# Optimization experiments

Measured on AMD Instinct MI355X. Metric: run time of the kernel, lower is better.

## Reference

```python
import jax, jax.numpy as jnp
import numpy as np

N, NUM_MEM, HIDDEN = 131072, 1024, 256
TEMPERATURE = 0.5
EPS = 1e-12  # matches F.normalize default eps


def setup_inputs() -> dict:
    key = jax.random.key(0)
    k1, k2 = jax.random.split(key)
    x = jax.random.normal(k1, (N, HIDDEN), dtype=jnp.float32)
    # xavier_uniform-style init for the memory bank
    limit = float(np.sqrt(6.0 / (NUM_MEM + HIDDEN)))
    memories = jax.random.uniform(k2, (NUM_MEM, HIDDEN), dtype=jnp.float32,
                                  minval=-limit, maxval=limit)
    return {"x": x, "memories": memories}


def reference(x, memories):
    # cosine similarity: normalize both sides, then QK^T
    x_norm = x / jnp.maximum(jnp.linalg.norm(x, axis=-1, keepdims=True), EPS)
    mem_norm = memories / jnp.maximum(
        jnp.linalg.norm(memories, axis=-1, keepdims=True), EPS)
    logits = jnp.einsum('nd,md->nm', x_norm, mem_norm) / TEMPERATURE
    weight = jax.nn.softmax(logits, axis=-1)        # [N, num_memories]
    read = jnp.einsum('nm,md->nd', weight, memories)  # weighted memory read
    return read
```

## Files before the change

kernel.cpp:

```cpp
#include <hip/hip_runtime.h>
#include <hip/hip_bf16.h>
#include <stdint.h>

#define HIDDEN 256
#define NMEM   1024
#define NTILES 32
#define LOG2E  1.44269504088896340736f

typedef __attribute__((ext_vector_type(8)))  short bf16x8;
typedef __attribute__((ext_vector_type(16))) float f32x16;
typedef unsigned short ushort_t;
typedef unsigned int   uint_t;

__device__ __forceinline__ ushort_t f2bf(float f) {
  uint_t u = __builtin_bit_cast(uint_t, f);
  u += 0x7FFFu + ((u >> 16) & 1u);
  return (ushort_t)(u >> 16);
}

__device__ __forceinline__ void gload_lds16(const void* g, void* l) {
  __builtin_amdgcn_global_load_lds(
      (const __attribute__((address_space(1))) uint_t*)g,
      (__attribute__((address_space(3))) uint_t*)l, 16, 0, 0);
}

__global__ void prep_kernel(const float* __restrict__ mem,
                            ushort_t* __restrict__ wsm,
                            ushort_t* __restrict__ wsv) {
  const int m = blockIdx.x;
  const int k = threadIdx.x;
  float v = mem[m * HIDDEN + k];
  float ss = v * v;
  #pragma unroll
  for (int off = 1; off < 64; off <<= 1) ss += __shfl_xor(ss, off);
  __shared__ float red[4];
  if ((k & 63) == 0) red[k >> 6] = ss;
  __syncthreads();
  const float tot = red[0] + red[1] + red[2] + red[3];
  const float inv = 1.0f / fmaxf(sqrtf(tot), 1e-12f);
  const ushort_t hn = f2bf(v * inv);
  const ushort_t hv = f2bf(v);
  const int t = m >> 5, mr = m & 31;
  wsm[t * 8192 + mr * 256 + (((k >> 3) ^ (mr & 7)) << 3) + (k & 7)] = hn;
  wsv[t * 8192 + k * 32  + (((mr >> 3) ^ ((k >> 1) & 3)) << 3) + (mr & 7)] = hv;
}

__global__ __launch_bounds__(512, 2) void mem_kernel(
    const float* __restrict__ x, const ushort_t* __restrict__ wsm,
    const ushort_t* __restrict__ wsv, float* __restrict__ out) {
  __shared__ __align__(16) char lds[65536];
  const int tid  = threadIdx.x;
  const int lane = tid & 63;
  const int wave = tid >> 6;
  const int col  = lane & 31;
  const int hi   = lane >> 5;
  const int row0 = blockIdx.x * 256 + wave * 32;
  const char* gm = (const char*)wsm;
  const char* gv = (const char*)wsv;

  auto stage = [&](int t, int buf) {
    const int bb = buf << 15;
    const int go = t * 16384;
    #pragma unroll
    for (int r = 0; r < 2; ++r) {
      const int o = wave * 2048 + r * 1024;
      gload_lds16(gm + go + o + lane * 16, lds + bb + o);
      gload_lds16(gv + go + o + lane * 16, lds + bb + 16384 + o);
    }
  };

  stage(0, 0);

  bf16x8 xb[16];
  float ss = 0.f;
  const float* xr = x + (size_t)(row0 + col) * HIDDEN + hi * 8;
  #pragma unroll
  for (int ks = 0; ks < 16; ++ks) {
    float4 a = *(const float4*)(xr + ks * 16);
    float4 b = *(const float4*)(xr + ks * 16 + 4);
    ss += a.x*a.x + a.y*a.y + a.z*a.z + a.w*a.w
        + b.x*b.x + b.y*b.y + b.z*b.z + b.w*b.w;
    xb[ks][0] = (short)f2bf(a.x); xb[ks][1] = (short)f2bf(a.y);
    xb[ks][2] = (short)f2bf(a.z); xb[ks][3] = (short)f2bf(a.w);
    xb[ks][4] = (short)f2bf(b.x); xb[ks][5] = (short)f2bf(b.y);
    xb[ks][6] = (short)f2bf(b.z); xb[ks][7] = (short)f2bf(b.w);
  }
  ss += __shfl_xor(ss, 32);
  const float myscale = (2.0f * LOG2E) / fmaxf(sqrtf(ss), 1e-12f);

  const f32x16 zz = {0.f,0.f,0.f,0.f, 0.f,0.f,0.f,0.f,
                     0.f,0.f,0.f,0.f, 0.f,0.f,0.f,0.f};
  f32x16 o8[8];
  #pragma unroll
  for (int i = 0; i < 8; ++i) o8[i] = zz;
  float den = 0.f;

  const int ck7 = col & 7;
  const int ck3 = (col >> 1) & 3;

  __syncthreads();

  for (int t = 0; t < NTILES; ++t) {
    const int mb = (t & 1) << 15;
    const int vb = mb + 16384;
    if (t < NTILES - 1) stage(t + 1, (t & 1) ^ 1);
    __builtin_amdgcn_s_setprio(1);

    const char* ab = lds + mb + col * 512;
    f32x16 s0 = zz, s1 = zz;
    #pragma unroll
    for (int ks2 = 0; ks2 < 8; ++ks2) {
      bf16x8 a0 = *(const bf16x8*)(ab + (((4*ks2 + hi)     ^ ck7) << 4));
      bf16x8 a1 = *(const bf16x8*)(ab + (((4*ks2 + 2 + hi) ^ ck7) << 4));
      s0 = __builtin_amdgcn_mfma_f32_32x32x16_bf16(a0, xb[2*ks2],   s0, 0,0,0);
      s1 = __builtin_amdgcn_mfma_f32_32x32x16_bf16(a1, xb[2*ks2+1], s1, 0,0,0);
    }

    float p[16];
    #pragma unroll
    for (int r = 0; r < 16; ++r) {
      const float pv = exp2f((s0[r] + s1[r]) * myscale);
      den += pv;
      p[r] = pv;
    }

    bf16x8 pa[2];
    #pragma unroll
    for (int ks = 0; ks < 2; ++ks) {
      const int b0 = ks * 8;
      uint_t w0 = (uint_t)f2bf(p[b0+0]) | ((uint_t)f2bf(p[b0+1]) << 16);
      uint_t w1 = (uint_t)f2bf(p[b0+2]) | ((uint_t)f2bf(p[b0+3]) << 16);
      uint_t w2 = (uint_t)f2bf(p[b0+4]) | ((uint_t)f2bf(p[b0+5]) << 16);
      uint_t w3 = (uint_t)f2bf(p[b0+6]) | ((uint_t)f2bf(p[b0+7]) << 16);
      asm("v_permlane32_swap_b32 %0, %1" : "+v"(w0), "+v"(w2));
      asm("v_permlane32_swap_b32 %0, %1" : "+v"(w1), "+v"(w3));
      uint4 u = {w0, w1, w2, w3};
      pa[ks] = __builtin_bit_cast(bf16x8, u);
    }

    const char* vrb = lds + vb + col * 64;
    #pragma unroll
    for (int ks = 0; ks < 2; ++ks) {
      const int cc = ((2*ks + hi) ^ ck3) << 4;
      #pragma unroll
      for (int d0 = 0; d0 < 8; ++d0) {
        bf16x8 vf = *(const bf16x8*)(vrb + d0 * 2048 + cc);
        o8[d0] = __builtin_amdgcn_mfma_f32_32x32x16_bf16(pa[ks], vf, o8[d0], 0,0,0);
      }
    }
    __builtin_amdgcn_s_setprio(0);
    __syncthreads();
  }

  den += __shfl_xor(den, 32);
  const float rden = 1.0f / den;
  float rdv[16];
  #pragma unroll
  for (int r = 0; r < 16; ++r)
    rdv[r] = __shfl(rden, (r & 3) + 8 * (r >> 2) + 4 * hi);

  float* op = out + (size_t)row0 * HIDDEN;
  #pragma unroll
  for (int d0 = 0; d0 < 8; ++d0) {
    #pragma unroll
    for (int r = 0; r < 16; ++r) {
      const int rw = (r & 3) + 8 * (r >> 2) + 4 * hi;
      op[(size_t)rw * HIDDEN + d0 * 32 + col] = o8[d0][r] * rdv[r];
    }
  }
}

extern "C" void kernel_launch(void* const* d_in, const int* in_sizes, int n_in,
                              void* d_out, int out_size, void* d_ws, size_t ws_size,
                              hipStream_t stream) {
  const float* x   = (const float*)d_in[0];
  const float* mem = (const float*)d_in[1];
  float* out = (float*)d_out;
  const int N = in_sizes[0] / HIDDEN;

  ushort_t* wsm = (ushort_t*)d_ws;
  ushort_t* wsv = wsm + NMEM * HIDDEN;

  prep_kernel<<<NMEM, HIDDEN, 0, stream>>>(mem, wsm, wsv);
  mem_kernel<<<N / 256, 512, 0, stream>>>(x, wsm, wsv, out);
}
```

Before: 381.4 us.

## Software-pipeline QK and PV across tiles with triple-buffered LDS

Restructures the main loop so each iteration runs the QK MFMAs for the current tile while issuing the PV MFMAs for the previous tile's packed probabilities. A third LDS buffer is added so the PV operands of the previous tile stay resident while the next tile is staged. The aim is to hide the exp/convert dependency between QK and PV. It also switches to the hardware packed bf16 convert instruction and splits the denominator into two accumulators. LDS grows to 96KB per block, which may break the two-blocks-per-CU occupancy target.

```diff
diff --git a/kernel.cpp b/kernel.cpp
--- a/kernel.cpp
+++ b/kernel.cpp
@@ -48,7 +48,7 @@
 __global__ __launch_bounds__(512, 2) void mem_kernel(
     const float* __restrict__ x, const ushort_t* __restrict__ wsm,
     const ushort_t* __restrict__ wsv, float* __restrict__ out) {
-  __shared__ __align__(16) char lds[65536];
+  __shared__ __align__(16) char lds[98304];
   const int tid  = threadIdx.x;
   const int lane = tid & 63;
   const int wave = tid >> 6;
@@ -58,8 +58,8 @@
   const char* gm = (const char*)wsm;
   const char* gv = (const char*)wsv;
 
-  auto stage = [&](int t, int buf) {
-    const int bb = buf << 15;
+  auto stage = [&](int t, int b) {
+    const int bb = b * 32768;
     const int go = t * 16384;
     #pragma unroll
     for (int r = 0; r < 2; ++r) {
@@ -93,21 +93,15 @@
   f32x16 o8[8];
   #pragma unroll
   for (int i = 0; i < 8; ++i) o8[i] = zz;
-  float den = 0.f;
+  float den0 = 0.f, den1 = 0.f;
+  bf16x8 pa[2];
 
   const int ck7 = col & 7;
   const int ck3 = (col >> 1) & 3;
 
-  __syncthreads();
-
-  for (int t = 0; t < NTILES; ++t) {
-    const int mb = (t & 1) << 15;
-    const int vb = mb + 16384;
-    if (t < NTILES - 1) stage(t + 1, (t & 1) ^ 1);
-    __builtin_amdgcn_s_setprio(1);
-
-    const char* ab = lds + mb + col * 512;
-    f32x16 s0 = zz, s1 = zz;
+  auto qk = [&](int qb, f32x16& s0, f32x16& s1) {
+    const char* ab = lds + qb * 32768 + col * 512;
+    s0 = zz; s1 = zz;
     #pragma unroll
     for (int ks2 = 0; ks2 < 8; ++ks2) {
       bf16x8 a0 = *(const bf16x8*)(ab + (((4*ks2 + hi)     ^ ck7) << 4));
@@ -115,30 +109,36 @@
       s0 = __builtin_amdgcn_mfma_f32_32x32x16_bf16(a0, xb[2*ks2],   s0, 0,0,0);
       s1 = __builtin_amdgcn_mfma_f32_32x32x16_bf16(a1, xb[2*ks2+1], s1, 0,0,0);
     }
-
-    float p[16];
-    #pragma unroll
-    for (int r = 0; r < 16; ++r) {
-      const float pv = exp2f((s0[r] + s1[r]) * myscale);
-      den += pv;
-      p[r] = pv;
-    }
-
-    bf16x8 pa[2];
+  };
+
+  auto pack = [&](const f32x16& s0, const f32x16& s1) {
     #pragma unroll
     for (int ks = 0; ks < 2; ++ks) {
       const int b0 = ks * 8;
-      uint_t w0 = (uint_t)f2bf(p[b0+0]) | ((uint_t)f2bf(p[b0+1]) << 16);
-      uint_t w1 = (uint_t)f2bf(p[b0+2]) | ((uint_t)f2bf(p[b0+3]) << 16);
-      uint_t w2 = (uint_t)f2bf(p[b0+4]) | ((uint_t)f2bf(p[b0+5]) << 16);
-      uint_t w3 = (uint_t)f2bf(p[b0+6]) | ((uint_t)f2bf(p[b0+7]) << 16);
+      const float e0 = exp2f((s0[b0+0] + s1[b0+0]) * myscale);
+      const float e1 = exp2f((s0[b0+1] + s1[b0+1]) * myscale);
+      const float e2 = exp2f((s0[b0+2] + s1[b0+2]) * myscale);
+      const float e3 = exp2f((s0[b0+3] + s1[b0+3]) * myscale);
+      const float e4 = exp2f((s0[b0+4] + s1[b0+4]) * myscale);
+      const float e5 = exp2f((s0[b0+5] + s1[b0+5]) * myscale);
+      const float e6 = exp2f((s0[b0+6] + s1[b0+6]) * myscale);
+      const float e7 = exp2f((s0[b0+7] + s1[b0+7]) * myscale);
+      den0 += (e0 + e1) + (e2 + e3);
+      den1 += (e4 + e5) + (e6 + e7);
+      uint_t w0, w1, w2, w3;
+      asm("v_cvt_pk_bf16_f32 %0, %1, %2" : "=v"(w0) : "v"(e0), "v"(e1));
+      asm("v_cvt_pk_bf16_f32 %0, %1, %2" : "=v"(w1) : "v"(e2), "v"(e3));
+      asm("v_cvt_pk_bf16_f32 %0, %1, %2" : "=v"(w2) : "v"(e4), "v"(e5));
+      asm("v_cvt_pk_bf16_f32 %0, %1, %2" : "=v"(w3) : "v"(e6), "v"(e7));
       asm("v_permlane32_swap_b32 %0, %1" : "+v"(w0), "+v"(w2));
       asm("v_permlane32_swap_b32 %0, %1" : "+v"(w1), "+v"(w3));
       uint4 u = {w0, w1, w2, w3};
       pa[ks] = __builtin_bit_cast(bf16x8, u);
     }
-
-    const char* vrb = lds + vb + col * 64;
+  };
+
+  auto pv = [&](int pb) {
+    const char* vrb = lds + pb * 32768 + 16384 + col * 64;
     #pragma unroll
     for (int ks = 0; ks < 2; ++ks) {
       const int cc = ((2*ks + hi) ^ ck3) << 4;
@@ -148,10 +148,37 @@
         o8[d0] = __builtin_amdgcn_mfma_f32_32x32x16_bf16(pa[ks], vf, o8[d0], 0,0,0);
       }
     }
+  };
+
+  auto iter = [&](int t, int qb, int pb, int sb, bool do_stage) {
+    if (do_stage) stage(t + 1, sb);
+    __builtin_amdgcn_s_setprio(1);
+    f32x16 s0, s1;
+    qk(qb, s0, s1);
+    pv(pb);
+    pack(s0, s1);
     __builtin_amdgcn_s_setprio(0);
     __syncthreads();
+  };
+
+  __syncthreads();
+
+  stage(1, 1);
+  __builtin_amdgcn_s_setprio(1);
+  { f32x16 s0, s1; qk(0, s0, s1); pack(s0, s1); }
+  __builtin_amdgcn_s_setprio(0);
+  __syncthreads();
+
+  #pragma unroll 1
+  for (int tb = 1; tb < 31; tb += 3) {
+    iter(tb,     1, 0, 2, true);
+    iter(tb + 1, 2, 1, 0, true);
+    iter(tb + 2, 0, 2, 1, true);
   }
-
+  iter(31, 1, 0, 0, false);
+  pv(1);
+
+  float den = den0 + den1;
   den += __shfl_xor(den, 32);
   const float rden = 1.0f / den;
   float rdv[16];
```

Measured after the change: 579.8 us. 52.0% more time.
